# Kernel optimization log

Hardware: AMD Instinct MI355X
Metric: run time of the kernel (lower is better)

## Reference

```python
import jax, jax.numpy as jnp
import numpy as np

DIM = 768
HEADS = 12


def setup_inputs() -> dict:
    key = jax.random.key(0)
    ks = jax.random.split(key, 7)
    bs, nmm, nv, na = 32, 256, 196, 60
    s = DIM ** -0.5
    return {
        "xmm": jax.random.normal(ks[0], (bs, nmm, DIM), jnp.float32),
        "xv": jax.random.normal(ks[1], (bs, nv, DIM), jnp.float32),
        "xa": jax.random.normal(ks[2], (bs, na, DIM), jnp.float32),
        "Wq": jax.random.normal(ks[3], (DIM, DIM), jnp.float32) * s,
        "Wkv": jax.random.normal(ks[4], (DIM, 2 * DIM), jnp.float32) * s,
        "Wproj": jax.random.normal(ks[5], (DIM, DIM), jnp.float32) * s,
        "bproj": jnp.zeros((DIM,), jnp.float32),
    }


def reference(xmm, xv, xa, Wq, Wkv, Wproj, bproj):
    bs, nmm, dim = xmm.shape
    hd = dim // HEADS
    scale = hd ** -0.5
    x_src = jnp.concatenate([xv, xa], axis=1)            # [bs, nv+na, dim]
    q = (xmm @ Wq).reshape(bs, nmm, HEADS, hd).transpose(0, 2, 1, 3)   # [b,h,q,d]
    kv = (x_src @ Wkv).reshape(bs, -1, 2, HEADS, hd).transpose(2, 0, 3, 1, 4)
    k, v = kv[0], kv[1]                                  # [b,h,k,d]
    attn = jax.nn.softmax(jnp.einsum('bhqd,bhkd->bhqk', q, k) * scale, axis=-1)
    out = jnp.einsum('bhqk,bhkd->bhqd', attn, v)
    out = out.transpose(0, 2, 1, 3).reshape(bs, nmm, dim)
    out = out @ Wproj + bproj
    return out, attn
```

## Files before the change

kernel.cpp:

```cpp
#include <hip/hip_runtime.h>


typedef __attribute__((ext_vector_type(8))) _Float16 f16x8;
typedef __attribute__((ext_vector_type(4))) _Float16 f16x4;
typedef __attribute__((ext_vector_type(4))) float    f32x4;

#define AS1 __attribute__((address_space(1)))
#define AS3 __attribute__((address_space(3)))

__device__ __forceinline__ void gload_lds16(const void* g, void* l) {
    void* gnc = const_cast<void*>(g);
    __builtin_amdgcn_global_load_lds((AS1 void*)gnc, (AS3 void*)l, 16, 0, 0);
}

__global__ __launch_bounds__(256) void prep_acts(const float* __restrict__ xmm,
                                                 const float* __restrict__ xv,
                                                 const float* __restrict__ xa,
                                                 _Float16* __restrict__ xmm16,
                                                 _Float16* __restrict__ xsrc16) {
    int id = blockIdx.x * 256 + threadIdx.x;
    float4 v;
    _Float16* dst;
    int off;
    if (id < 1572864) {
        v = ((const float4*)xmm)[id];
        dst = xmm16; off = id;
    } else {
        int t = id - 1572864;
        int c4 = t % 192;
        int r  = (t / 192) & 255;
        int b  = t / 49152;
        if (r < 196) v = ((const float4*)xv)[((long)b * 196 + r) * 192 + c4];
        else         v = ((const float4*)xa)[((long)b * 60 + (r - 196)) * 192 + c4];
        dst = xsrc16; off = t;
    }
    f16x4 h = { (_Float16)v.x, (_Float16)v.y, (_Float16)v.z, (_Float16)v.w };
    ((f16x4*)dst)[off] = h;
}

__global__ __launch_bounds__(256) void prep_weights(const float* __restrict__ Wq,
                                                    const float* __restrict__ Wkv,
                                                    const float* __restrict__ Wproj,
                                                    _Float16* __restrict__ WqT,
                                                    _Float16* __restrict__ WkvT,
                                                    _Float16* __restrict__ WprojT) {
    int id = blockIdx.x * 256 + threadIdx.x;
    if (id < 589824) {
        int k = id % 768, n = id / 768;
        WqT[id] = (_Float16)(0.125f * Wq[(long)k * 768 + n]);
        return;
    }
    id -= 589824;
    if (id < 1179648) {
        int k = id % 768, n = id / 768;
        WkvT[id] = (_Float16)Wkv[(long)k * 1536 + n];
        return;
    }
    id -= 1179648;
    if (id < 589824) {
        int k = id % 768, n = id / 768;
        WprojT[id] = (_Float16)Wproj[(long)k * 768 + n];
    }
}

template <int OUT_F32>
__device__ __forceinline__ void gemm_body(const _Float16* __restrict__ A,
                                          const _Float16* __restrict__ Bt,
                                          void* __restrict__ C,
                                          const float* __restrict__ bias,
                                          long bm, long bn, int N, int K) {
    __shared__ _Float16 As[128 * 64];
    __shared__ _Float16 Bs[128 * 64];

    const int tid  = threadIdx.x;
    const int wave = tid >> 6, lane = tid & 63;
    const int lrow = lane & 15, quad = lane >> 4;
    const int wm = (wave >> 1) * 64, wn = (wave & 1) * 64;

    f32x4 acc[4][4];
    const f32x4 fz = {0.f, 0.f, 0.f, 0.f};
#pragma unroll
    for (int mt = 0; mt < 4; ++mt)
#pragma unroll
        for (int nt = 0; nt < 4; ++nt) acc[mt][nt] = fz;

    for (int k0 = 0; k0 < K; k0 += 64) {
#pragma unroll
        for (int it = 0; it < 4; ++it) {
            int seg = tid + it * 256;
            int rr = seg >> 3, pp = seg & 7;
            int cc = ((pp ^ (rr & 7)) << 3);
            gload_lds16(A  + (bm + rr) * (long)K + k0 + cc, As + seg * 8);
            gload_lds16(Bt + (bn + rr) * (long)K + k0 + cc, Bs + seg * 8);
        }
        __syncthreads();
#pragma unroll
        for (int ks = 0; ks < 2; ++ks) {
            f16x8 af[4], bf[4];
#pragma unroll
            for (int mt = 0; mt < 4; ++mt) {
                int r = wm + mt * 16 + lrow;
                af[mt] = *(const f16x8*)(As + r * 64 + (((ks * 4 + quad) ^ (r & 7)) << 3));
            }
#pragma unroll
            for (int nt = 0; nt < 4; ++nt) {
                int r = wn + nt * 16 + lrow;
                bf[nt] = *(const f16x8*)(Bs + r * 64 + (((ks * 4 + quad) ^ (r & 7)) << 3));
            }
#pragma unroll
            for (int mt = 0; mt < 4; ++mt)
#pragma unroll
                for (int nt = 0; nt < 4; ++nt)
                    acc[mt][nt] = __builtin_amdgcn_mfma_f32_16x16x32_f16(
                        bf[nt], af[mt], acc[mt][nt], 0, 0, 0);
        }
        __syncthreads();
    }

#pragma unroll
    for (int mt = 0; mt < 4; ++mt) {
        long row = bm + wm + mt * 16 + lrow;
#pragma unroll
        for (int nt = 0; nt < 4; ++nt) {
            long col0 = bn + wn + nt * 16 + quad * 4;
            if (OUT_F32) {
                float4 b4 = *(const float4*)(bias + col0);
                float4 o = { acc[mt][nt][0] + b4.x, acc[mt][nt][1] + b4.y,
                             acc[mt][nt][2] + b4.z, acc[mt][nt][3] + b4.w };
                *(float4*)((float*)C + row * N + col0) = o;
            } else {
                f16x4 h = { (_Float16)acc[mt][nt][0], (_Float16)acc[mt][nt][1],
                            (_Float16)acc[mt][nt][2], (_Float16)acc[mt][nt][3] };
                *(f16x4*)((_Float16*)C + row * N + col0) = h;
            }
        }
    }
}

__global__ __launch_bounds__(256, 2)
void gemm_qkv(const _Float16* __restrict__ xmm16, const _Float16* __restrict__ xsrc16,
              const _Float16* __restrict__ WqT, const _Float16* __restrict__ WkvT,
              _Float16* __restrict__ Q16, _Float16* __restrict__ KV16) {
    const int bx = blockIdx.x;
    const long bm = (long)blockIdx.y * 128;
    if (bx < 6) gemm_body<0>(xmm16,  WqT,  (void*)Q16,  nullptr, bm, (long)bx * 128,       768,  768);
    else        gemm_body<0>(xsrc16, WkvT, (void*)KV16, nullptr, bm, (long)(bx - 6) * 128, 1536, 768);
}

__global__ __launch_bounds__(256, 2)
void gemm_proj(const _Float16* __restrict__ O16, const _Float16* __restrict__ WprojT,
               float* __restrict__ out, const float* __restrict__ bias) {
    gemm_body<1>(O16, WprojT, (void*)out, bias, (long)blockIdx.y * 128, (long)blockIdx.x * 128, 768, 768);
}

__global__ __launch_bounds__(256, 2)
void attn_kernel(const _Float16* __restrict__ Qg, const _Float16* __restrict__ KVg,
                 float* __restrict__ attn_out, _Float16* __restrict__ Og) {
    __shared__ _Float16 sh[32768];
    _Float16* Ks = sh;
    _Float16* Vt = sh + 16384;
    _Float16* Ps = sh;

    const int tid  = threadIdx.x;
    const int wave = tid >> 6, lane = tid & 63;
    const int lrow = lane & 15, quad = lane >> 4;
    const int qb = blockIdx.x, h = blockIdx.y, b = blockIdx.z;
    const long qrow0 = (long)b * 256 + qb * 64;
    const long krow0 = (long)b * 256;

    f16x8 aq[2];
#pragma unroll
    for (int ks = 0; ks < 2; ++ks)
        aq[ks] = *(const f16x8*)(Qg + (qrow0 + wave * 16 + lrow) * 768 + h * 64 + ks * 32 + quad * 8);

#pragma unroll
    for (int it = 0; it < 8; ++it) {
        int seg = tid + it * 256;
        int rr = seg >> 3, pp = seg & 7;
        int cc = ((pp ^ (rr & 7)) << 3);
        gload_lds16(KVg + (krow0 + rr) * 1536 + h * 64 + cc, Ks + seg * 8);
    }
#pragma unroll
    for (int it = 0; it < 8; ++it) {
        int seg = tid + it * 256;
        int key = seg >> 3, d0 = (seg & 7) * 8;
        f16x8 v = *(const f16x8*)(KVg + (krow0 + key) * 1536 + 768 + h * 64 + d0);
#pragma unroll
        for (int i = 0; i < 8; ++i) {
            int d = d0 + i;
            Vt[d * 256 + ((((key >> 3) ^ (d & 7)) << 3) | (key & 7))] = v[i];
        }
    }
    __syncthreads();

    f32x4 sacc[16];
    const f32x4 fz = {0.f, 0.f, 0.f, 0.f};
#pragma unroll
    for (int nt = 0; nt < 16; ++nt) sacc[nt] = fz;
#pragma unroll
    for (int ks = 0; ks < 2; ++ks) {
#pragma unroll
        for (int nt = 0; nt < 16; ++nt) {
            int r = nt * 16 + lrow;
            f16x8 bk = *(const f16x8*)(Ks + r * 64 + (((ks * 4 + quad) ^ (r & 7)) << 3));
            sacc[nt] = __builtin_amdgcn_mfma_f32_16x16x32_f16(bk, aq[ks], sacc[nt], 0, 0, 0);
        }
    }

    float m = -1e30f;
#pragma unroll
    for (int nt = 0; nt < 16; ++nt)
#pragma unroll
        for (int j = 0; j < 4; ++j) m = fmaxf(m, sacc[nt][j]);
    m = fmaxf(m, __shfl_xor(m, 16));
    m = fmaxf(m, __shfl_xor(m, 32));
    float s = 0.f;
#pragma unroll
    for (int nt = 0; nt < 16; ++nt)
#pragma unroll
        for (int j = 0; j < 4; ++j) {
            float p = __expf(sacc[nt][j] - m);
            sacc[nt][j] = p; s += p;
        }
    s += __shfl_xor(s, 16);
    s += __shfl_xor(s, 32);
    const float li = 1.f / s;

    __syncthreads();

    const long abase = (((long)b * 12 + h) * 256 + qb * 64) * 256;
    const int q = wave * 16 + lrow;
#pragma unroll
    for (int nt = 0; nt < 16; ++nt) {
        float4 o = { sacc[nt][0] * li, sacc[nt][1] * li, sacc[nt][2] * li, sacc[nt][3] * li };
        *(float4*)(attn_out + abase + (long)q * 256 + nt * 16 + quad * 4) = o;
        f16x4 hp = { (_Float16)o.x, (_Float16)o.y, (_Float16)o.z, (_Float16)o.w };
        int blk = nt * 2 + (quad >> 1);
        *(f16x4*)(Ps + q * 256 + ((blk ^ (q & 7)) << 3) + ((quad & 1) << 2)) = hp;
    }
    __syncthreads();

    f32x4 oacc[4];
#pragma unroll
    for (int nt = 0; nt < 4; ++nt) oacc[nt] = fz;
#pragma unroll
    for (int ks = 0; ks < 8; ++ks) {
        int pr = wave * 16 + lrow;
        f16x8 ap = *(const f16x8*)(Ps + pr * 256 + (((ks * 4 + quad) ^ (pr & 7)) << 3));
#pragma unroll
        for (int nt = 0; nt < 4; ++nt) {
            int d = nt * 16 + lrow;
            f16x8 bv = *(const f16x8*)(Vt + d * 256 + (((ks * 4 + quad) ^ (d & 7)) << 3));
            oacc[nt] = __builtin_amdgcn_mfma_f32_16x16x32_f16(bv, ap, oacc[nt], 0, 0, 0);
        }
    }
#pragma unroll
    for (int nt = 0; nt < 4; ++nt) {
        f16x4 ho = { (_Float16)oacc[nt][0], (_Float16)oacc[nt][1],
                     (_Float16)oacc[nt][2], (_Float16)oacc[nt][3] };
        *(f16x4*)(Og + (qrow0 + wave * 16 + lrow) * 768 + h * 64 + nt * 16 + quad * 4) = ho;
    }
}

extern "C" void kernel_launch(void* const* d_in, const int* in_sizes, int n_in,
                              void* d_out, int out_size, void* d_ws, size_t ws_size,
                              hipStream_t stream) {
    const float* xmm   = (const float*)d_in[0];
    const float* xv    = (const float*)d_in[1];
    const float* xa    = (const float*)d_in[2];
    const float* Wq    = (const float*)d_in[3];
    const float* Wkv   = (const float*)d_in[4];
    const float* Wproj = (const float*)d_in[5];
    const float* bproj = (const float*)d_in[6];

    float* out  = (float*)d_out;
    float* attn = out + 6291456;

    char* ws = (char*)d_ws;
    _Float16* xmm16  = (_Float16*)(ws);
    _Float16* xsrc16 = (_Float16*)(ws + 12582912);
    _Float16* WqT    = (_Float16*)(ws + 25165824);
    _Float16* WkvT   = (_Float16*)(ws + 26345472);
    _Float16* WprojT = (_Float16*)(ws + 28704768);
    _Float16* Q16    = (_Float16*)(ws + 29884416);
    _Float16* KV16   = (_Float16*)(ws + 42467328);
    _Float16* O16    = xmm16;

    prep_acts   <<<12288, 256, 0, stream>>>(xmm, xv, xa, xmm16, xsrc16);
    prep_weights<<<9216,  256, 0, stream>>>(Wq, Wkv, Wproj, WqT, WkvT, WprojT);

    gemm_qkv<<<dim3(18, 64), 256, 0, stream>>>(xmm16, xsrc16, WqT, WkvT, Q16, KV16);

    attn_kernel<<<dim3(4, 12, 32), 256, 0, stream>>>(Q16, KV16, attn, O16);

    gemm_proj<<<dim3(6, 64), 256, 0, stream>>>(O16, WprojT, out, bproj);
}
```

Before: 298.9 us.

## Emit transposed V from QKV GEMM and read K/V directly from global in attention

Result: slower. 308.2 us (+3.1%).

```diff
diff --git a/kernel.cpp b/kernel.cpp
--- a/kernel.cpp
+++ b/kernel.cpp
@@ -9,42 +9,41 @@
 #define AS3 __attribute__((address_space(3)))
 
 __device__ __forceinline__ void gload_lds16(const void* g, void* l) {
-    void* gnc = const_cast<void*>(g);
-    __builtin_amdgcn_global_load_lds((AS1 void*)gnc, (AS3 void*)l, 16, 0, 0);
-}
-
-__global__ __launch_bounds__(256) void prep_acts(const float* __restrict__ xmm,
-                                                 const float* __restrict__ xv,
-                                                 const float* __restrict__ xa,
-                                                 _Float16* __restrict__ xmm16,
-                                                 _Float16* __restrict__ xsrc16) {
+    __builtin_amdgcn_global_load_lds((AS1 void*)const_cast<void*>(g), (AS3 void*)l, 16, 0, 0);
+}
+
+__global__ __launch_bounds__(256) void prep_all(const float* __restrict__ xmm,
+                                                const float* __restrict__ xv,
+                                                const float* __restrict__ xa,
+                                                const float* __restrict__ Wq,
+                                                const float* __restrict__ Wkv,
+                                                const float* __restrict__ Wproj,
+                                                _Float16* __restrict__ xmm16,
+                                                _Float16* __restrict__ xsrc16,
+                                                _Float16* __restrict__ WqT,
+                                                _Float16* __restrict__ WkvT,
+                                                _Float16* __restrict__ WprojT) {
     int id = blockIdx.x * 256 + threadIdx.x;
-    float4 v;
-    _Float16* dst;
-    int off;
-    if (id < 1572864) {
-        v = ((const float4*)xmm)[id];
-        dst = xmm16; off = id;
-    } else {
-        int t = id - 1572864;
-        int c4 = t % 192;
-        int r  = (t / 192) & 255;
-        int b  = t / 49152;
-        if (r < 196) v = ((const float4*)xv)[((long)b * 196 + r) * 192 + c4];
-        else         v = ((const float4*)xa)[((long)b * 60 + (r - 196)) * 192 + c4];
-        dst = xsrc16; off = t;
-    }
-    f16x4 h = { (_Float16)v.x, (_Float16)v.y, (_Float16)v.z, (_Float16)v.w };
-    ((f16x4*)dst)[off] = h;
-}
-
-__global__ __launch_bounds__(256) void prep_weights(const float* __restrict__ Wq,
-                                                    const float* __restrict__ Wkv,
-                                                    const float* __restrict__ Wproj,
-                                                    _Float16* __restrict__ WqT,
-                                                    _Float16* __restrict__ WkvT,
-                                                    _Float16* __restrict__ WprojT) {
-    int id = blockIdx.x * 256 + threadIdx.x;
+    if (id < 3145728) {
+        float4 v;
+        _Float16* dst; int off;
+        if (id < 1572864) {
+            v = ((const float4*)xmm)[id];
+            dst = xmm16; off = id;
+        } else {
+            int t = id - 1572864;
+            int c4 = t % 192;
+            int r  = (t / 192) & 255;
+            int b  = t / 49152;
+            if (r < 196) v = ((const float4*)xv)[((long)b * 196 + r) * 192 + c4];
+            else         v = ((const float4*)xa)[((long)b * 60 + (r - 196)) * 192 + c4];
+            dst = xsrc16; off = t;
+        }
+        f16x4 h = { (_Float16)v.x, (_Float16)v.y, (_Float16)v.z, (_Float16)v.w };
+        ((f16x4*)dst)[off] = h;
+        return;
+    }
+    id -= 3145728;
     if (id < 589824) {
         int k = id % 768, n = id / 768;
         WqT[id] = (_Float16)(0.125f * Wq[(long)k * 768 + n]);
@@ -63,7 +62,9 @@
     }
 }
 
-template <int OUT_F32>
+enum { EPI_F16_ROW = 0, EPI_F32_BIAS = 1, EPI_F16_VT = 2 };
+
+template <int EPI>
 __device__ __forceinline__ void gemm_body(const _Float16* __restrict__ A,
                                           const _Float16* __restrict__ Bt,
                                           void* __restrict__ C,
@@ -110,28 +111,49 @@
 #pragma unroll
             for (int mt = 0; mt < 4; ++mt)
 #pragma unroll
-                for (int nt = 0; nt < 4; ++nt)
-                    acc[mt][nt] = __builtin_amdgcn_mfma_f32_16x16x32_f16(
-                        bf[nt], af[mt], acc[mt][nt], 0, 0, 0);
+                for (int nt = 0; nt < 4; ++nt) {
+                    if (EPI == EPI_F16_VT)
+                        acc[mt][nt] = __builtin_amdgcn_mfma_f32_16x16x32_f16(
+                            af[mt], bf[nt], acc[mt][nt], 0, 0, 0);
+                    else
+                        acc[mt][nt] = __builtin_amdgcn_mfma_f32_16x16x32_f16(
+                            bf[nt], af[mt], acc[mt][nt], 0, 0, 0);
+                }
         }
         __syncthreads();
     }
 
-#pragma unroll
-    for (int mt = 0; mt < 4; ++mt) {
-        long row = bm + wm + mt * 16 + lrow;
-#pragma unroll
-        for (int nt = 0; nt < 4; ++nt) {
-            long col0 = bn + wn + nt * 16 + quad * 4;
-            if (OUT_F32) {
-                float4 b4 = *(const float4*)(bias + col0);
-                float4 o = { acc[mt][nt][0] + b4.x, acc[mt][nt][1] + b4.y,
-                             acc[mt][nt][2] + b4.z, acc[mt][nt][3] + b4.w };
-                *(float4*)((float*)C + row * N + col0) = o;
-            } else {
+    if (EPI == EPI_F16_VT) {
+        const long b = bm >> 8;
+        const int key0 = (int)(bm & 255);
+#pragma unroll
+        for (int mt = 0; mt < 4; ++mt) {
+            int key = key0 + wm + mt * 16 + quad * 4;
+#pragma unroll
+            for (int nt = 0; nt < 4; ++nt) {
+                long nd = bn + wn + nt * 16 + lrow;
                 f16x4 h = { (_Float16)acc[mt][nt][0], (_Float16)acc[mt][nt][1],
                             (_Float16)acc[mt][nt][2], (_Float16)acc[mt][nt][3] };
-                *(f16x4*)((_Float16*)C + row * N + col0) = h;
+                *(f16x4*)((_Float16*)C + (b * 768 + nd) * 256 + key) = h;
+            }
+        }
+    } else {
+#pragma unroll
+        for (int mt = 0; mt < 4; ++mt) {
+            long row = bm + wm + mt * 16 + lrow;
+#pragma unroll
+            for (int nt = 0; nt < 4; ++nt) {
+                long col0 = bn + wn + nt * 16 + quad * 4;
+                if (EPI == EPI_F32_BIAS) {
+                    float4 b4 = *(const float4*)(bias + col0);
+                    float4 o = { acc[mt][nt][0] + b4.x, acc[mt][nt][1] + b4.y,
+                                 acc[mt][nt][2] + b4.z, acc[mt][nt][3] + b4.w };
+                    *(float4*)((float*)C + row * N + col0) = o;
+                } else {
+                    f16x4 h = { (_Float16)acc[mt][nt][0], (_Float16)acc[mt][nt][1],
+                                (_Float16)acc[mt][nt][2], (_Float16)acc[mt][nt][3] };
+                    *(f16x4*)((_Float16*)C + row * N + col0) = h;
+                }
             }
         }
     }
@@ -140,26 +162,30 @@
 __global__ __launch_bounds__(256, 2)
 void gemm_qkv(const _Float16* __restrict__ xmm16, const _Float16* __restrict__ xsrc16,
               const _Float16* __restrict__ WqT, const _Float16* __restrict__ WkvT,
-              _Float16* __restrict__ Q16, _Float16* __restrict__ KV16) {
+              _Float16* __restrict__ Q16, _Float16* __restrict__ K16,
+              _Float16* __restrict__ Vt16) {
     const int bx = blockIdx.x;
     const long bm = (long)blockIdx.y * 128;
-    if (bx < 6) gemm_body<0>(xmm16,  WqT,  (void*)Q16,  nullptr, bm, (long)bx * 128,       768,  768);
-    else        gemm_body<0>(xsrc16, WkvT, (void*)KV16, nullptr, bm, (long)(bx - 6) * 128, 1536, 768);
+    if (bx < 6)
+        gemm_body<EPI_F16_ROW>(xmm16, WqT, (void*)Q16, nullptr, bm, (long)bx * 128, 768, 768);
+    else if (bx < 12)
+        gemm_body<EPI_F16_ROW>(xsrc16, WkvT, (void*)K16, nullptr, bm, (long)(bx - 6) * 128, 768, 768);
+    else
+        gemm_body<EPI_F16_VT>(xsrc16, WkvT + 768L * 768, (void*)Vt16, nullptr, bm, (long)(bx - 12) * 128, 256, 768);
 }
 
 __global__ __launch_bounds__(256, 2)
 void gemm_proj(const _Float16* __restrict__ O16, const _Float16* __restrict__ WprojT,
                float* __restrict__ out, const float* __restrict__ bias) {
-    gemm_body<1>(O16, WprojT, (void*)out, bias, (long)blockIdx.y * 128, (long)blockIdx.x * 128, 768, 768);
-}
-
-__global__ __launch_bounds__(256, 2)
-void attn_kernel(const _Float16* __restrict__ Qg, const _Float16* __restrict__ KVg,
-                 float* __restrict__ attn_out, _Float16* __restrict__ Og) {
-    __shared__ _Float16 sh[32768];
-    _Float16* Ks = sh;
-    _Float16* Vt = sh + 16384;
-    _Float16* Ps = sh;
+    gemm_body<EPI_F32_BIAS>(O16, WprojT, (void*)out, bias,
+                            (long)blockIdx.y * 128, (long)blockIdx.x * 128, 768, 768);
+}
+
+__global__ __launch_bounds__(256, 3)
+void attn_kernel(const _Float16* __restrict__ Qg, const _Float16* __restrict__ Kg,
+                 const _Float16* __restrict__ Vt, float* __restrict__ attn_out,
+                 _Float16* __restrict__ Og) {
+    __shared__ _Float16 Ps[64 * 256];
 
     const int tid  = threadIdx.x;
     const int wave = tid >> 6, lane = tid & 63;
@@ -167,32 +193,13 @@
     const int qb = blockIdx.x, h = blockIdx.y, b = blockIdx.z;
     const long qrow0 = (long)b * 256 + qb * 64;
     const long krow0 = (long)b * 256;
+    const long vbase = ((long)b * 768 + h * 64) * 256;
 
     f16x8 aq[2];
 #pragma unroll
     for (int ks = 0; ks < 2; ++ks)
         aq[ks] = *(const f16x8*)(Qg + (qrow0 + wave * 16 + lrow) * 768 + h * 64 + ks * 32 + quad * 8);
 
-#pragma unroll
-    for (int it = 0; it < 8; ++it) {
-        int seg = tid + it * 256;
-        int rr = seg >> 3, pp = seg & 7;
-        int cc = ((pp ^ (rr & 7)) << 3);
-        gload_lds16(KVg + (krow0 + rr) * 1536 + h * 64 + cc, Ks + seg * 8);
-    }
-#pragma unroll
-    for (int it = 0; it < 8; ++it) {
-        int seg = tid + it * 256;
-        int key = seg >> 3, d0 = (seg & 7) * 8;
-        f16x8 v = *(const f16x8*)(KVg + (krow0 + key) * 1536 + 768 + h * 64 + d0);
-#pragma unroll
-        for (int i = 0; i < 8; ++i) {
-            int d = d0 + i;
-            Vt[d * 256 + ((((key >> 3) ^ (d & 7)) << 3) | (key & 7))] = v[i];
-        }
-    }
-    __syncthreads();
-
     f32x4 sacc[16];
     const f32x4 fz = {0.f, 0.f, 0.f, 0.f};
 #pragma unroll
@@ -201,8 +208,7 @@
     for (int ks = 0; ks < 2; ++ks) {
 #pragma unroll
         for (int nt = 0; nt < 16; ++nt) {
-            int r = nt * 16 + lrow;
-            f16x8 bk = *(const f16x8*)(Ks + r * 64 + (((ks * 4 + quad) ^ (r & 7)) << 3));
+            f16x8 bk = *(const f16x8*)(Kg + (krow0 + nt * 16 + lrow) * 768 + h * 64 + ks * 32 + quad * 8);
             sacc[nt] = __builtin_amdgcn_mfma_f32_16x16x32_f16(bk, aq[ks], sacc[nt], 0, 0, 0);
         }
     }
@@ -226,8 +232,6 @@
     s += __shfl_xor(s, 32);
     const float li = 1.f / s;
 
-    __syncthreads();
-
     const long abase = (((long)b * 12 + h) * 256 + qb * 64) * 256;
     const int q = wave * 16 + lrow;
 #pragma unroll
@@ -235,22 +239,22 @@
         float4 o = { sacc[nt][0] * li, sacc[nt][1] * li, sacc[nt][2] * li, sacc[nt][3] * li };
         *(float4*)(attn_out + abase + (long)q * 256 + nt * 16 + quad * 4) = o;
         f16x4 hp = { (_Float16)o.x, (_Float16)o.y, (_Float16)o.z, (_Float16)o.w };
-        int blk = nt * 2 + (quad >> 1);
-        *(f16x4*)(Ps + q * 256 + ((blk ^ (q & 7)) << 3) + ((quad & 1) << 2)) = hp;
-    }
-    __syncthreads();
+        int key  = nt * 16 + quad * 4;
+        int phys = (key >> 3) ^ (q & 31);
+        *(f16x4*)(Ps + q * 256 + (phys << 3) + (key & 7)) = hp;
+    }
+    __asm__ __volatile__("s_waitcnt lgkmcnt(0)" ::: "memory");
 
     f32x4 oacc[4];
 #pragma unroll
     for (int nt = 0; nt < 4; ++nt) oacc[nt] = fz;
 #pragma unroll
     for (int ks = 0; ks < 8; ++ks) {
-        int pr = wave * 16 + lrow;
-        f16x8 ap = *(const f16x8*)(Ps + pr * 256 + (((ks * 4 + quad) ^ (pr & 7)) << 3));
+        int kq = ks * 4 + quad;
+        f16x8 ap = *(const f16x8*)(Ps + q * 256 + ((kq ^ (q & 31)) << 3));
 #pragma unroll
         for (int nt = 0; nt < 4; ++nt) {
-            int d = nt * 16 + lrow;
-            f16x8 bv = *(const f16x8*)(Vt + d * 256 + (((ks * 4 + quad) ^ (d & 7)) << 3));
+            f16x8 bv = *(const f16x8*)(Vt + vbase + (nt * 16 + lrow) * 256 + ks * 32 + quad * 8);
             oacc[nt] = __builtin_amdgcn_mfma_f32_16x16x32_f16(bv, ap, oacc[nt], 0, 0, 0);
         }
     }
@@ -283,15 +287,16 @@
     _Float16* WkvT   = (_Float16*)(ws + 26345472);
     _Float16* WprojT = (_Float16*)(ws + 28704768);
     _Float16* Q16    = (_Float16*)(ws + 29884416);
-    _Float16* KV16   = (_Float16*)(ws + 42467328);
+    _Float16* K16    = (_Float16*)(ws + 42467328);
+    _Float16* Vt16   = (_Float16*)(ws + 55050240);
     _Float16* O16    = xmm16;
 
-    prep_acts   <<<12288, 256, 0, stream>>>(xmm, xv, xa, xmm16, xsrc16);
-    prep_weights<<<9216,  256, 0, stream>>>(Wq, Wkv, Wproj, WqT, WkvT, WprojT);
-
-    gemm_qkv<<<dim3(18, 64), 256, 0, stream>>>(xmm16, xsrc16, WqT, WkvT, Q16, KV16);
-
-    attn_kernel<<<dim3(4, 12, 32), 256, 0, stream>>>(Q16, KV16, attn, O16);
+    prep_all<<<21504, 256, 0, stream>>>(xmm, xv, xa, Wq, Wkv, Wproj,
+                                        xmm16, xsrc16, WqT, WkvT, WprojT);
+
+    gemm_qkv<<<dim3(18, 64), 256, 0, stream>>>(xmm16, xsrc16, WqT, WkvT, Q16, K16, Vt16);
+
+    attn_kernel<<<dim3(4, 12, 32), 256, 0, stream>>>(Q16, K16, Vt16, attn, O16);
 
     gemm_proj<<<dim3(6, 64), 256, 0, stream>>>(O16, WprojT, out, bproj);
 }
```
